# Optimization experiments

Measured on AMD Instinct MI355X. Metric: run time of the kernel, lower is better.

Reference implementation:

```python
import jax, jax.numpy as jnp
import numpy as np
import math

F = 32                      # multiplicity per irrep (l0dim = l1dim = l2dim)
NUMBASIS = 8
RCUT = 4.0
BESSEL_END = 5.0
AVG_NEIGHBORS = 25.0
N_NODES = 10000
N_EDGES = 250000
HIDDEN = 64
FEAT = 9 * F                # (1+3+5) components per channel

# uvu tensor-product paths (l_in1, l_edge, l_out) allowed by l/parity selection rules
PATHS = [(0,0,0),(0,1,1),(0,2,2),(1,0,1),(1,1,0),(1,1,2),(1,2,1),(2,0,2),(2,1,1),(2,2,0),(2,2,2)]
_cnt = {}
for (_,_,k) in PATHS:
    _cnt[k] = _cnt.get(k, 0) + 1
# e3nn path weights: irrep_normalization='component', path_normalization='element' (num_elements(uvu)=mul_in2=1)
PATH_W = [math.sqrt((2*k+1) / _cnt[k]) for (_,_,k) in PATHS]

def _su2_cg(j1, j2, j3, m1, m2, m3):
    if m1 + m2 != m3:
        return 0.0
    f = math.factorial
    pref = math.sqrt((2*j3+1) * f(j1+j2-j3) * f(j1-j2+j3) * f(-j1+j2+j3) / f(j1+j2+j3+1))
    pref *= math.sqrt(f(j3+m3) * f(j3-m3) * f(j1-m1) * f(j1+m1) * f(j2-m2) * f(j2+m2))
    s = 0.0
    for k in range(0, j1+j2-j3+1):
        d = [k, j1+j2-j3-k, j1-m1-k, j2+m2-k, j3-j2+m1+k, j3-j1-m2+k]
        if min(d) < 0:
            continue
        s += (-1)**k / (f(d[0])*f(d[1])*f(d[2])*f(d[3])*f(d[4])*f(d[5]))
    return pref * s

def _q(l):
    # complex->real SH change of basis (e3nn convention)
    q = np.zeros((2*l+1, 2*l+1), dtype=np.complex128)
    for m in range(-l, 0):
        q[l+m, l+abs(m)] = 1/math.sqrt(2)
        q[l+m, l-abs(m)] = -1j/math.sqrt(2)
    q[l, l] = 1.0
    for m in range(1, l+1):
        q[l+m, l+abs(m)] = (-1)**m/math.sqrt(2)
        q[l+m, l-abs(m)] = 1j*(-1)**m/math.sqrt(2)
    return (-1j)**l * q

def _w3j(l1, l2, l3):
    C = np.zeros((2*l1+1, 2*l2+1, 2*l3+1))
    for m1 in range(-l1, l1+1):
        for m2 in range(-l2, l2+1):
            for m3 in range(-l3, l3+1):
                C[l1+m1, l2+m2, l3+m3] = _su2_cg(l1, l2, l3, m1, m2, m3)
    W = np.einsum('ij,kl,mn,ikm->jln', _q(l1), _q(l2), np.conj(_q(l3)), C.astype(np.complex128))
    Wr, Wi = np.real(W), np.imag(W)
    W = Wr if np.linalg.norm(Wr) >= np.linalg.norm(Wi) else Wi
    return (W / np.linalg.norm(W)).astype(np.float32)   # unit-Frobenius real 3j, as in e3nn

W3J = {p: _w3j(*p) for p in PATHS}

def _bessel(d):
    # soft_one_hot_linspace(d, 0, 5, 8, basis='bessel', cutoff=True)
    t = d / BESSEL_END
    n = jnp.arange(1, NUMBASIS + 1, dtype=d.dtype)
    safe_t = jnp.where(t > 0, t, 1.0)
    out = math.sqrt(2.0 / BESSEL_END) * jnp.sin(n * jnp.pi * t[:, None]) / safe_t[:, None]
    return out * (((t > 0) & (t < 1)).astype(d.dtype))[:, None]

def _poly_cutoff(d):
    u = d / RCUT                      # p = 6
    env = 1.0 - 6.0 * u**5 + 5.0 * u**6
    return env * (d < RCUT).astype(d.dtype)

def _sph(unit):
    # component-normalized real spherical harmonics l=0,1,2 on unit vectors
    x, y, z = unit[:, 0], unit[:, 1], unit[:, 2]
    y0 = jnp.ones_like(x)[:, None]
    y1 = math.sqrt(3.0) * jnp.stack([y, z, x], axis=-1)
    y2 = jnp.stack([
        math.sqrt(15.0) * x * y,
        math.sqrt(15.0) * y * z,
        (math.sqrt(5.0) / 2.0) * (3.0 * z * z - 1.0),
        math.sqrt(15.0) * x * z,
        (math.sqrt(15.0) / 2.0) * (x * x - y * y),
    ], axis=-1)
    return (y0, y1, y2)

def _forward(nodes, pos, src, dst, w1, b1, w2, b2):
    neighbors = nodes[src]                                    # [E, 9F] gather
    posvec = pos[src] - pos[dst]                              # [E, 3]
    dist = jnp.sqrt(jnp.sum(posvec * posvec, axis=1))         # [E]
    h = jax.nn.silu(_bessel(dist) @ w1 + b1)                  # [E, 64]
    radial = (h @ w2 + b2) * _poly_cutoff(dist)[:, None]      # [E, 11F]
    w = radial.reshape(-1, len(PATHS), F)                     # [E, P, F]
    unit = posvec / jnp.maximum(dist, 1e-12)[:, None]
    ys = _sph(unit)                                           # ([E,1],[E,3],[E,5])
    x0 = neighbors[:, :F].reshape(-1, F, 1)
    x1 = neighbors[:, F:4*F].reshape(-1, F, 3)
    x2 = neighbors[:, 4*F:].reshape(-1, F, 5)
    xs = (x0, x1, x2)
    outs = [0.0, 0.0, 0.0]
    for p, (i, j, k) in enumerate(PATHS):
        Wp = jnp.asarray(W3J[(i, j, k)])                      # [di, dj, dk]
        msg = jnp.einsum('abc,eua,eb,eu->euc', Wp, xs[i], ys[j], w[:, p, :])
        outs[k] = outs[k] + PATH_W[p] * msg
    messages = jnp.concatenate([o.reshape(o.shape[0], -1) for o in outs], axis=1)  # [E, 9F]
    agg = jax.ops.segment_sum(messages, dst, num_segments=N_NODES)
    return agg / math.sqrt(AVG_NEIGHBORS)

def setup_inputs():
    key = jax.random.key(0)
    ks = jax.random.split(key, 6)
    nodes = jax.random.normal(ks[0], (N_NODES, FEAT), dtype=jnp.float32)
    pos = jax.random.normal(ks[1], (N_NODES, 3), dtype=jnp.float32)
    src = jax.random.randint(ks[2], (N_EDGES,), 0, N_NODES)
    dst = jax.random.randint(ks[3], (N_EDGES,), 0, N_NODES)
    w1 = jax.random.normal(ks[4], (NUMBASIS, HIDDEN), dtype=jnp.float32) / math.sqrt(NUMBASIS)
    b1 = jnp.zeros((HIDDEN,), jnp.float32)
    w2 = jax.random.normal(ks[5], (HIDDEN, len(PATHS)*F), dtype=jnp.float32) / math.sqrt(HIDDEN)
    b2 = jnp.zeros((len(PATHS)*F,), jnp.float32)
    return {"nodes": nodes, "pos": pos, "src": src, "dst": dst, "w1": w1, "b1": b1, "w2": w2, "b2": b2}

def reference(nodes, pos, src, dst, w1, b1, w2, b2):
    return _forward(nodes, pos, src, dst, w1, b1, w2, b2)
```

## Files before the change

kernel.cpp:

```cpp
#include <hip/hip_runtime.h>
#include <hip/hip_bf16.h>
#include <cmath>
#include <complex>

#define TPB 256
#define WPB 4
#define NM 115
#define NW3J 363
#define MPITCH 116
#define RPITCH 388
#define W2FN 22528
#define SCAN_T 1024
#define NBUCK 256

typedef __attribute__((ext_vector_type(8))) short bf16x8;
typedef __attribute__((ext_vector_type(4))) float f32x4;

namespace {

double fct(int n){ double r=1; for(int i=2;i<=n;i++) r*=i; return r; }

double su2_cg(int j1,int j2,int j3,int m1,int m2,int m3){
  if(m1+m2!=m3) return 0.0;
  double pref = std::sqrt((2*j3+1)*fct(j1+j2-j3)*fct(j1-j2+j3)*fct(-j1+j2+j3)/fct(j1+j2+j3+1));
  pref *= std::sqrt(fct(j3+m3)*fct(j3-m3)*fct(j1-m1)*fct(j1+m1)*fct(j2-m2)*fct(j2+m2));
  double s=0;
  for(int k=0;k<=j1+j2-j3;k++){
    int d0=k, d1=j1+j2-j3-k, d2=j1-m1-k, d3=j2+m2-k, d4=j3-j2+m1+k, d5=j3-j1-m2+k;
    if(d0<0||d1<0||d2<0||d3<0||d4<0||d5<0) continue;
    double t = 1.0/(fct(d0)*fct(d1)*fct(d2)*fct(d3)*fct(d4)*fct(d5));
    s += (k&1)? -t : t;
  }
  return pref*s;
}

typedef std::complex<double> cd;

void qmat(int l, cd q[5][5]){
  for(int i=0;i<5;i++) for(int j=0;j<5;j++) q[i][j] = cd(0,0);
  const double is2 = 1.0/std::sqrt(2.0);
  for(int m=-l;m<0;m++){ q[l+m][l-m] = cd(is2,0); q[l+m][l+m] = cd(0,-is2); }
  q[l][l] = cd(1,0);
  for(int m=1;m<=l;m++){ double sg = (m&1)? -1.0: 1.0; q[l+m][l+m] = cd(sg*is2,0); q[l+m][l-m] = cd(0, sg*is2); }
  cd ph(1,0), mi(0,-1);
  for(int t=0;t<l;t++) ph *= mi;
  for(int i=0;i<5;i++) for(int j=0;j<5;j++) q[i][j] *= ph;
}

void w3j_calc(int l1,int l2,int l3,double* out){
  int n1=2*l1+1,n2=2*l2+1,n3=2*l3+1;
  double C[5][5][5] = {};
  for(int m1=-l1;m1<=l1;m1++)for(int m2=-l2;m2<=l2;m2++)for(int m3=-l3;m3<=l3;m3++)
    C[l1+m1][l2+m2][l3+m3] = su2_cg(l1,l2,l3,m1,m2,m3);
  cd q1[5][5], q2[5][5], q3[5][5];
  qmat(l1,q1); qmat(l2,q2); qmat(l3,q3);
  double wr[125], wi[125];
  double nr=0, ni=0;
  for(int a=0;a<n1;a++)for(int b=0;b<n2;b++)for(int c=0;c<n3;c++){
    cd s(0,0);
    for(int i=0;i<n1;i++)for(int k=0;k<n2;k++)for(int m=0;m<n3;m++)
      s += q1[i][a]*q2[k][b]*std::conj(q3[m][c])*C[i][k][m];
    int idx = (a*n2+b)*n3+c;
    wr[idx]=s.real(); wi[idx]=s.imag();
    nr += s.real()*s.real(); ni += s.imag()*s.imag();
  }
  bool useR = std::sqrt(nr) >= std::sqrt(ni);
  double nn = std::sqrt(useR? nr: ni);
  for(int q=0;q<n1*n2*n3;q++) out[q] = (useR? wr[q]: wi[q])/nn;
}

struct UploadArg {
  float w3j[NW3J];
  unsigned int meta[NM];
};

UploadArg g_upload;

struct BuildInit {
  BuildInit(){
    const int P[11][3] = {{0,0,0},{0,1,1},{0,2,2},{1,0,1},{1,1,0},{1,1,2},
                          {1,2,1},{2,0,2},{2,1,1},{2,2,0},{2,2,2}};
    const int cnt[3] = {3,4,4};
    const int AO[3] = {0,1,4};
    int off = 0, t = 0;
    for(int p=0;p<11;p++){
      int i=P[p][0], j=P[p][1], k=P[p][2];
      int na=2*i+1, nb=2*j+1, nc=2*k+1;
      double W[125];
      w3j_calc(i,j,k,W);
      double pw = std::sqrt((2.0*k+1.0)/(double)cnt[k]);
      for(int q=0;q<na*nb*nc;q++) g_upload.w3j[off+q] = (float)(W[q]*pw);
      for(int a=0;a<na;a++)
        for(int c=0;c<nc;c++)
          g_upload.meta[t++] = (unsigned)((off + a*nb*nc + c) | (nc<<10) | (nb<<14) | (AO[j]<<18));
      off += na*nb*nc;
    }
  }
};
BuildInit g_build_init;

}


__global__ void count_repack_kernel(const int* __restrict__ dst, int* __restrict__ counts,
                                    const float* __restrict__ w2,
                                    unsigned short* __restrict__ w2f, int E){
  int i = blockIdx.x*blockDim.x + threadIdx.x;
  if(i < W2FN){
    int jj = i & 7;
    int lane = (i>>3) & 63;
    int kk = (i>>9) & 1;
    int t  = i>>10;
    int n = t*16 + (lane & 15);
    int k = kk*32 + ((lane>>4)&3)*8 + jj;
    unsigned ub = __float_as_uint(w2[k*352 + n]);
    ub = (ub + 0x7fffu + ((ub>>16)&1u)) >> 16;
    w2f[i] = (unsigned short)ub;
  }
  if(i < E) atomicAdd(&counts[dst[i]], 1);
}

__global__ __launch_bounds__(SCAN_T) void megascan_kernel(const int* __restrict__ counts,
                                                          int* __restrict__ off,
                                                          int* __restrict__ cursor,
                                                          int* __restrict__ bcur, int NN){
  __shared__ int part[SCAN_T];
  __shared__ int lh[NBUCK];
  int t = threadIdx.x;
  if(t < NBUCK) lh[t] = 0;
  __syncthreads();
  int C = (NN + SCAN_T - 1)/SCAN_T;
  int base = t*C;
  int lim = min(base+C, NN);
  int s = 0;
  for(int i=base;i<lim;i++){
    int c = counts[i];
    s += c;
    atomicAdd(&lh[min(c, NBUCK-1)], 1);
  }
  part[t] = s;
  __syncthreads();
  for(int d=1; d<SCAN_T; d<<=1){
    int v = (t>=d)? part[t-d] : 0;
    __syncthreads();
    part[t] += v;
    __syncthreads();
  }
  int run = part[t] - s;
  for(int i=base;i<lim;i++){ off[i]=run; cursor[i]=run; run += counts[i]; }
  if(t == SCAN_T-1) off[NN] = part[t];
  __syncthreads();
  if(t == 0){
    int r = 0;
    for(int b=0;b<NBUCK;b++){ bcur[b] = r; r += lh[b]; }
  }
}

__global__ void scatter_kernel(const int* __restrict__ dst, const int* __restrict__ counts,
                               int* __restrict__ cursor, int* __restrict__ bcur,
                               int* __restrict__ node_order, int* __restrict__ eid,
                               int NN, int E){
  int i = blockIdx.x*blockDim.x + threadIdx.x;
  if(i < NN){
    int p = atomicAdd(&bcur[min(counts[i], NBUCK-1)], 1);
    node_order[p] = i;
  }
  if(i < E){
    int p = atomicAdd(&cursor[dst[i]], 1);
    eid[p] = i;
  }
}


__global__ __launch_bounds__(TPB) void node_kernel(
    const float* __restrict__ nodes,
    const float* __restrict__ pos,
    const int* __restrict__ src,
    const int* __restrict__ node_order,
    const int* __restrict__ offp,
    const int* __restrict__ eid,
    const unsigned short* __restrict__ w2f,
    const float* __restrict__ w1,
    const float* __restrict__ b1,
    const float* __restrict__ b2,
    float* __restrict__ outp,
    int NN, UploadArg up)
{
  __shared__ alignas(16) float s_w3j[NW3J];
  __shared__ alignas(16) float s_w1[512];
  __shared__ alignas(16) float s_b1[64];
  __shared__ alignas(16) float s_b2[352];
  __shared__ alignas(16) unsigned short s_h[WPB][16*68];
  __shared__ alignas(16) float s_M[WPB][16*MPITCH];
  __shared__ alignas(16) float s_rad[WPB][16*RPITCH];

  const int tid  = threadIdx.x;
  const int wid  = tid >> 6;
  const int lane = tid & 63;
  const int q    = lane >> 4;
  const int i    = lane & 15;
  const int u    = lane & 31;
  const int half = lane >> 5;

  for(int t=tid; t<NW3J; t+=TPB) s_w3j[t] = up.w3j[t];
  for(int t=tid; t<512; t+=TPB)  s_w1[t]  = w1[t];
  for(int t=tid; t<352; t+=TPB)  s_b2[t]  = b2[t];
  if(tid < 64) s_b1[tid] = b1[tid];
  __syncthreads();

  const int nidx   = blockIdx.x*WPB + wid;
  const bool active = nidx < NN;
  const int node   = active ? node_order[nidx] : 0;
  const int start  = offp[node];
  const int deg    = active ? (offp[node+1] - start) : 0;

  const float dpx = pos[node*3+0], dpy = pos[node*3+1], dpz = pos[node*3+2];

  float accv[9];
  #pragma unroll
  for(int k=0;k<9;k++) accv[k] = 0.0f;

  char* hbytes = (char*)&s_h[wid][0];
  float* Mw    = &s_M[wid][0];
  float* radw  = &s_rad[wid][0];
  const uint4* w2f4 = (const uint4*)w2f;

  constexpr int PI_[11]   = {0,0,0,1,1,1,1,2,2,2,2};
  constexpr int PK_[11]   = {0,1,2,1,0,2,1,2,1,0,2};
  constexpr int TOFF_[11] = {0,1,4,9,18,21,36,45,70,85,90};
  constexpr int AO_[3]    = {0,1,4};

  const int nch = (deg + 15) >> 4;

  for(int ch=0; ch<nch; ch++){
    int ei = ch*16 + i;
    bool v = ei < deg;
    int eg = v ? eid[start+ei] : 0;
    int se = v ? src[eg] : node;
    float px = pos[se*3+0]-dpx, py = pos[se*3+1]-dpy, pz = pos[se*3+2]-dpz;
    float d2 = px*px + py*py + pz*pz;
    float d  = v ? sqrtf(d2) : 1e9f;
    float inv = 1.0f/fmaxf(d, 1e-12f);
    float x = px*inv, y = py*inv, z = pz*inv;
    float yv[9];
    yv[0]=1.0f;
    yv[1]=1.7320508075688772f*y;
    yv[2]=1.7320508075688772f*z;
    yv[3]=1.7320508075688772f*x;
    yv[4]=3.872983346207417f*x*y;
    yv[5]=3.872983346207417f*y*z;
    yv[6]=1.118033988749895f*(3.0f*z*z-1.0f);
    yv[7]=3.872983346207417f*x*z;
    yv[8]=1.9364916731037085f*(x*x-y*y);
    float bes[8];
    {
      float tt = d * 0.2f;
      float st = (tt > 0.0f) ? tt : 1.0f;
      float msk = (tt > 0.0f && tt < 1.0f) ? 1.0f : 0.0f;
      float ang = 3.14159265358979323846f * tt;
      float s1 = __sinf(ang), c1 = __cosf(ang);
      float kk2 = 0.6324555320336759f * msk / st;
      float c2 = 2.0f*c1;
      float sp = 0.0f, sc = s1;
      bes[0] = kk2*s1;
      #pragma unroll
      for(int n=1;n<8;n++){ float sn = c2*sc - sp; sp = sc; sc = sn; bes[n] = kk2*sn; }
    }
    float cut;
    {
      float uu = d*0.25f;
      float u2 = uu*uu;
      float u5 = u2*u2*uu;
      float env = 1.0f - 6.0f*u5 + 5.0f*u5*uu;
      cut = (d < 4.0f) ? env : 0.0f;
    }

    unsigned hp[8];
    #pragma unroll
    for(int s=0;s<16;s++){
      int j = q*16 + s;
      float a = s_b1[j];
      #pragma unroll
      for(int k=0;k<8;k++) a += bes[k]*s_w1[k*64+j];
      float sg = 1.0f/(1.0f + __expf(-a));
      float h = a*sg;
      unsigned ub = __float_as_uint(h);
      ub = (ub + 0x7fffu + ((ub>>16)&1u)) >> 16;
      if(s & 1) hp[s>>1] |= ub<<16; else hp[s>>1] = ub;
    }
    {
      uint2* wp = (uint2*)(hbytes + i*136 + q*32);
      wp[0] = make_uint2(hp[0],hp[1]);
      wp[1] = make_uint2(hp[2],hp[3]);
      wp[2] = make_uint2(hp[4],hp[5]);
      wp[3] = make_uint2(hp[6],hp[7]);
    }

    for(int s5=0; s5<29; s5++){
      int t = q + 4*s5;
      if(t < NM){
        unsigned md = up.meta[t];
        int woff = md & 1023;
        int nc   = (md>>10) & 15;
        int nb   = (md>>14) & 15;
        int boff = (md>>18) & 15;
        float sm = 0.0f;
        for(int b=0;b<nb;b++) sm += s_w3j[woff + b*nc] * yv[boff + b];
        Mw[i*MPITCH + t] = sm;
      }
    }

    float cut4[4];
    #pragma unroll
    for(int r=0;r<4;r++) cut4[r] = __shfl(cut, 4*q + r);

    __threadfence_block();

    union UA { uint2 u2[2]; bf16x8 v; };
    UA A0, A1;
    {
      const char* ab = hbytes + i*136 + q*16;
      A0.u2[0] = *(const uint2*)(ab);
      A0.u2[1] = *(const uint2*)(ab + 8);
      A1.u2[0] = *(const uint2*)(ab + 64);
      A1.u2[1] = *(const uint2*)(ab + 72);
    }

    #pragma unroll 2
    for(int p=0;p<11;p++){
      #pragma unroll
      for(int hv=0;hv<2;hv++){
        int t = 2*p + hv;
        union UB { uint4 u4; bf16x8 v; } B0, B1;
        B0.u4 = w2f4[(t*2+0)*64 + lane];
        B1.u4 = w2f4[(t*2+1)*64 + lane];
        f32x4 c = {0.f,0.f,0.f,0.f};
        c = __builtin_amdgcn_mfma_f32_16x16x32_bf16(A0.v, B0.v, c, 0,0,0);
        c = __builtin_amdgcn_mfma_f32_16x16x32_bf16(A1.v, B1.v, c, 0,0,0);
        float bias = s_b2[p*32 + hv*16 + i];
        #pragma unroll
        for(int r=0;r<4;r++){
          radw[(4*q+r)*RPITCH + (hv*16+i)*12 + p] = (c[r] + bias) * cut4[r];
        }
      }
    }

    __threadfence_block();

    for(int jj=0; jj<8; jj++){
      if(ch*16 + 2*jj >= deg) break;
      int e = 2*jj + half;
      int seE = __shfl(se, e);
      const float* nr = nodes + (long)seE*288;
      float xv[9];
      xv[0] = nr[u];
      #pragma unroll
      for(int c=0;c<3;c++) xv[1+c] = nr[32 + u*3 + c];
      #pragma unroll
      for(int c=0;c<5;c++) xv[4+c] = nr[128 + u*5 + c];
      const float* rp = radw + e*RPITCH + u*12;
      float4 r0 = *(const float4*)(rp);
      float4 r1 = *(const float4*)(rp+4);
      float4 r2 = *(const float4*)(rp+8);
      float wr[12] = {r0.x,r0.y,r0.z,r0.w, r1.x,r1.y,r1.z,r1.w, r2.x,r2.y,r2.z,r2.w};
      const float* Me = Mw + e*MPITCH;
      #pragma unroll
      for(int p=0;p<11;p++){
        const int na = 2*PI_[p]+1;
        const int nc = 2*PK_[p]+1;
        const int ai = AO_[PI_[p]], ko = AO_[PK_[p]];
        float w = wr[p];
        #pragma unroll
        for(int a=0;a<na;a++){
          float xw = xv[ai+a]*w;
          #pragma unroll
          for(int c=0;c<nc;c++) accv[ko+c] += xw * Me[TOFF_[p] + a*nc + c];
        }
      }
    }
  }

  #pragma unroll
  for(int k=0;k<9;k++) accv[k] += __shfl_xor(accv[k], 32);

  if(active && lane < 32){
    float* ob = outp + (long)node*288;
    ob[u] = 0.2f*accv[0];
    #pragma unroll
    for(int c=0;c<3;c++) ob[32 + u*3 + c] = 0.2f*accv[1+c];
    #pragma unroll
    for(int c=0;c<5;c++) ob[128 + u*5 + c] = 0.2f*accv[4+c];
  }
}


extern "C" void kernel_launch(void* const* d_in, const int* in_sizes, int n_in,
                              void* d_out, int out_size, void* d_ws, size_t ws_size,
                              hipStream_t stream) {
  const float* nodes = (const float*)d_in[0];
  const float* pos   = (const float*)d_in[1];
  const int* src = (const int*)d_in[2];
  const int* dst = (const int*)d_in[3];
  const float* w1 = (const float*)d_in[4];
  const float* b1 = (const float*)d_in[5];
  const float* w2 = (const float*)d_in[6];
  const float* b2 = (const float*)d_in[7];

  const int E  = in_sizes[2];
  const int NN = in_sizes[0] / 288;
  float* outp = (float*)d_out;

  unsigned short* w2f = (unsigned short*)d_ws;
  int* counts     = (int*)(w2f + W2FN);
  int* offp       = counts + NN;
  int* cursor     = offp + NN + 1;
  int* bcur       = cursor + NN;
  int* node_order = bcur + NBUCK;
  int* eid        = node_order + NN;

  hipMemsetAsync(counts, 0, (size_t)NN*sizeof(int), stream);

  int g1 = (max(E, W2FN) + 255)/256;
  count_repack_kernel<<<g1, 256, 0, stream>>>(dst, counts, w2, w2f, E);
  megascan_kernel<<<1, SCAN_T, 0, stream>>>(counts, offp, cursor, bcur, NN);
  int g2 = (max(E, NN) + 255)/256;
  scatter_kernel<<<g2, 256, 0, stream>>>(dst, counts, cursor, bcur, node_order, eid, NN, E);

  int nblocks = (NN + WPB - 1)/WPB;
  node_kernel<<<nblocks, TPB, 0, stream>>>(nodes, pos, src, node_order, offp, eid,
                                           w2f, w1, b1, b2, outp, NN, g_upload);
}
```

Before: 638.7 us.

## Consume MFMA radial weights in registers, drop radial LDS staging

The radial MLP output is now used straight from the MFMA accumulator registers instead of being written to a per-wave LDS buffer and read back. The tensor-product contraction is regrouped so each lane handles 4 edges × 16 channels, using a transposed M layout that is read with float4 loads. The LDS footprint shrinks and launch bounds ask for 3 blocks per CU. In exchange, block-wide __syncthreads replace per-wave fences, so every wave in a block runs as many chunks as the highest-degree wave, and each lane loads node features for 4 edges.

```diff
diff --git a/kernel.cpp b/kernel.cpp
--- a/kernel.cpp
+++ b/kernel.cpp
@@ -7,8 +7,6 @@
 #define WPB 4
 #define NM 115
 #define NW3J 363
-#define MPITCH 116
-#define RPITCH 388
 #define W2FN 22528
 #define SCAN_T 1024
 #define NBUCK 256
@@ -172,7 +170,7 @@
 }
 
 
-__global__ __launch_bounds__(TPB) void node_kernel(
+__global__ __launch_bounds__(TPB, 3) void node_kernel(
     const float* __restrict__ nodes,
     const float* __restrict__ pos,
     const int* __restrict__ src,
@@ -191,38 +189,44 @@
   __shared__ alignas(16) float s_b1[64];
   __shared__ alignas(16) float s_b2[352];
   __shared__ alignas(16) unsigned short s_h[WPB][16*68];
-  __shared__ alignas(16) float s_M[WPB][16*MPITCH];
-  __shared__ alignas(16) float s_rad[WPB][16*RPITCH];
+  __shared__ alignas(16) float s_MT[WPB][NM*16];
+  __shared__ int s_deg[WPB];
 
   const int tid  = threadIdx.x;
   const int wid  = tid >> 6;
   const int lane = tid & 63;
   const int q    = lane >> 4;
   const int i    = lane & 15;
-  const int u    = lane & 31;
-  const int half = lane >> 5;
 
   for(int t=tid; t<NW3J; t+=TPB) s_w3j[t] = up.w3j[t];
   for(int t=tid; t<512; t+=TPB)  s_w1[t]  = w1[t];
   for(int t=tid; t<352; t+=TPB)  s_b2[t]  = b2[t];
   if(tid < 64) s_b1[tid] = b1[tid];
-  __syncthreads();
 
   const int nidx   = blockIdx.x*WPB + wid;
   const bool active = nidx < NN;
   const int node   = active ? node_order[nidx] : 0;
   const int start  = offp[node];
   const int deg    = active ? (offp[node+1] - start) : 0;
+  if(lane == 0) s_deg[wid] = deg;
+  __syncthreads();
+
+  int degmax = s_deg[0];
+  #pragma unroll
+  for(int w=1;w<WPB;w++) degmax = max(degmax, s_deg[w]);
+  const int nch_blk  = (degmax + 15) >> 4;
+  const int nch_self = (deg + 15) >> 4;
 
   const float dpx = pos[node*3+0], dpy = pos[node*3+1], dpz = pos[node*3+2];
 
-  float accv[9];
+  float acc[2][9];
   #pragma unroll
-  for(int k=0;k<9;k++) accv[k] = 0.0f;
+  for(int hv=0;hv<2;hv++)
+    #pragma unroll
+    for(int k=0;k<9;k++) acc[hv][k] = 0.0f;
 
   char* hbytes = (char*)&s_h[wid][0];
-  float* Mw    = &s_M[wid][0];
-  float* radw  = &s_rad[wid][0];
+  float* MwT   = &s_MT[wid][0];
   const uint4* w2f4 = (const uint4*)w2f;
 
   constexpr int PI_[11]   = {0,0,0,1,1,1,1,2,2,2,2};
@@ -230,166 +234,177 @@
   constexpr int TOFF_[11] = {0,1,4,9,18,21,36,45,70,85,90};
   constexpr int AO_[3]    = {0,1,4};
 
-  const int nch = (deg + 15) >> 4;
-
-  for(int ch=0; ch<nch; ch++){
-    int ei = ch*16 + i;
-    bool v = ei < deg;
-    int eg = v ? eid[start+ei] : 0;
-    int se = v ? src[eg] : node;
-    float px = pos[se*3+0]-dpx, py = pos[se*3+1]-dpy, pz = pos[se*3+2]-dpz;
-    float d2 = px*px + py*py + pz*pz;
-    float d  = v ? sqrtf(d2) : 1e9f;
-    float inv = 1.0f/fmaxf(d, 1e-12f);
-    float x = px*inv, y = py*inv, z = pz*inv;
-    float yv[9];
-    yv[0]=1.0f;
-    yv[1]=1.7320508075688772f*y;
-    yv[2]=1.7320508075688772f*z;
-    yv[3]=1.7320508075688772f*x;
-    yv[4]=3.872983346207417f*x*y;
-    yv[5]=3.872983346207417f*y*z;
-    yv[6]=1.118033988749895f*(3.0f*z*z-1.0f);
-    yv[7]=3.872983346207417f*x*z;
-    yv[8]=1.9364916731037085f*(x*x-y*y);
-    float bes[8];
-    {
-      float tt = d * 0.2f;
-      float st = (tt > 0.0f) ? tt : 1.0f;
-      float msk = (tt > 0.0f && tt < 1.0f) ? 1.0f : 0.0f;
-      float ang = 3.14159265358979323846f * tt;
-      float s1 = __sinf(ang), c1 = __cosf(ang);
-      float kk2 = 0.6324555320336759f * msk / st;
-      float c2 = 2.0f*c1;
-      float sp = 0.0f, sc = s1;
-      bes[0] = kk2*s1;
+  for(int ch=0; ch<nch_blk; ch++){
+    const bool mine = (ch < nch_self);
+    float cut = 0.0f;
+    int   se  = node;
+
+    if(mine){
+      int ei = ch*16 + i;
+      bool v = ei < deg;
+      int eg = v ? eid[start+ei] : 0;
+      se = v ? src[eg] : node;
+      float px = pos[se*3+0]-dpx, py = pos[se*3+1]-dpy, pz = pos[se*3+2]-dpz;
+      float d2 = px*px + py*py + pz*pz;
+      float d  = v ? sqrtf(d2) : 1e9f;
+      float inv = 1.0f/fmaxf(d, 1e-12f);
+      float x = px*inv, y = py*inv, z = pz*inv;
+      float yv[9];
+      yv[0]=1.0f;
+      yv[1]=1.7320508075688772f*y;
+      yv[2]=1.7320508075688772f*z;
+      yv[3]=1.7320508075688772f*x;
+      yv[4]=3.872983346207417f*x*y;
+      yv[5]=3.872983346207417f*y*z;
+      yv[6]=1.118033988749895f*(3.0f*z*z-1.0f);
+      yv[7]=3.872983346207417f*x*z;
+      yv[8]=1.9364916731037085f*(x*x-y*y);
+      float bes[8];
+      {
+        float tt = d * 0.2f;
+        float st = (tt > 0.0f) ? tt : 1.0f;
+        float msk = (tt > 0.0f && tt < 1.0f) ? 1.0f : 0.0f;
+        float ang = 3.14159265358979323846f * tt;
+        float s1 = __sinf(ang), c1 = __cosf(ang);
+        float kk2 = 0.6324555320336759f * msk / st;
+        float c2 = 2.0f*c1;
+        float sp = 0.0f, sc = s1;
+        bes[0] = kk2*s1;
+        #pragma unroll
+        for(int n=1;n<8;n++){ float sn = c2*sc - sp; sp = sc; sc = sn; bes[n] = kk2*sn; }
+      }
+      {
+        float uu = d*0.25f;
+        float u2 = uu*uu;
+        float u5 = u2*u2*uu;
+        float env = 1.0f - 6.0f*u5 + 5.0f*u5*uu;
+        cut = (d < 4.0f) ? env : 0.0f;
+      }
+
+      unsigned hp[8];
       #pragma unroll
-      for(int n=1;n<8;n++){ float sn = c2*sc - sp; sp = sc; sc = sn; bes[n] = kk2*sn; }
-    }
-    float cut;
-    {
-      float uu = d*0.25f;
-      float u2 = uu*uu;
-      float u5 = u2*u2*uu;
-      float env = 1.0f - 6.0f*u5 + 5.0f*u5*uu;
-      cut = (d < 4.0f) ? env : 0.0f;
-    }
-
-    unsigned hp[8];
-    #pragma unroll
-    for(int s=0;s<16;s++){
-      int j = q*16 + s;
-      float a = s_b1[j];
+      for(int s=0;s<16;s++){
+        int j = q*16 + s;
+        float a = s_b1[j];
+        #pragma unroll
+        for(int k=0;k<8;k++) a += bes[k]*s_w1[k*64+j];
+        float sg = 1.0f/(1.0f + __expf(-a));
+        float h = a*sg;
+        unsigned ub = __float_as_uint(h);
+        ub = (ub + 0x7fffu + ((ub>>16)&1u)) >> 16;
+        if(s & 1) hp[s>>1] |= ub<<16; else hp[s>>1] = ub;
+      }
+      {
+        uint2* wp = (uint2*)(hbytes + i*136 + q*32);
+        wp[0] = make_uint2(hp[0],hp[1]);
+        wp[1] = make_uint2(hp[2],hp[3]);
+        wp[2] = make_uint2(hp[4],hp[5]);
+        wp[3] = make_uint2(hp[6],hp[7]);
+      }
+
+      for(int s5=0; s5<29; s5++){
+        int t = q + 4*s5;
+        if(t < NM){
+          unsigned md = up.meta[t];
+          int woff = md & 1023;
+          int nc   = (md>>10) & 15;
+          int nb   = (md>>14) & 15;
+          int boff = (md>>18) & 15;
+          float sm = 0.0f;
+          for(int b=0;b<nb;b++) sm += s_w3j[woff + b*nc] * yv[boff + b];
+          MwT[t*16 + i] = sm;
+        }
+      }
+    }
+
+    __syncthreads();
+
+    if(mine){
+      float cut4[4];
+      int   se4[4];
       #pragma unroll
-      for(int k=0;k<8;k++) a += bes[k]*s_w1[k*64+j];
-      float sg = 1.0f/(1.0f + __expf(-a));
-      float h = a*sg;
-      unsigned ub = __float_as_uint(h);
-      ub = (ub + 0x7fffu + ((ub>>16)&1u)) >> 16;
-      if(s & 1) hp[s>>1] |= ub<<16; else hp[s>>1] = ub;
-    }
-    {
-      uint2* wp = (uint2*)(hbytes + i*136 + q*32);
-      wp[0] = make_uint2(hp[0],hp[1]);
-      wp[1] = make_uint2(hp[2],hp[3]);
-      wp[2] = make_uint2(hp[4],hp[5]);
-      wp[3] = make_uint2(hp[6],hp[7]);
-    }
-
-    for(int s5=0; s5<29; s5++){
-      int t = q + 4*s5;
-      if(t < NM){
-        unsigned md = up.meta[t];
-        int woff = md & 1023;
-        int nc   = (md>>10) & 15;
-        int nb   = (md>>14) & 15;
-        int boff = (md>>18) & 15;
-        float sm = 0.0f;
-        for(int b=0;b<nb;b++) sm += s_w3j[woff + b*nc] * yv[boff + b];
-        Mw[i*MPITCH + t] = sm;
-      }
-    }
-
-    float cut4[4];
-    #pragma unroll
-    for(int r=0;r<4;r++) cut4[r] = __shfl(cut, 4*q + r);
-
-    __threadfence_block();
-
-    union UA { uint2 u2[2]; bf16x8 v; };
-    UA A0, A1;
-    {
-      const char* ab = hbytes + i*136 + q*16;
-      A0.u2[0] = *(const uint2*)(ab);
-      A0.u2[1] = *(const uint2*)(ab + 8);
-      A1.u2[0] = *(const uint2*)(ab + 64);
-      A1.u2[1] = *(const uint2*)(ab + 72);
-    }
-
-    #pragma unroll 2
-    for(int p=0;p<11;p++){
-      #pragma unroll
-      for(int hv=0;hv<2;hv++){
-        int t = 2*p + hv;
-        union UB { uint4 u4; bf16x8 v; } B0, B1;
-        B0.u4 = w2f4[(t*2+0)*64 + lane];
-        B1.u4 = w2f4[(t*2+1)*64 + lane];
-        f32x4 c = {0.f,0.f,0.f,0.f};
-        c = __builtin_amdgcn_mfma_f32_16x16x32_bf16(A0.v, B0.v, c, 0,0,0);
-        c = __builtin_amdgcn_mfma_f32_16x16x32_bf16(A1.v, B1.v, c, 0,0,0);
-        float bias = s_b2[p*32 + hv*16 + i];
+      for(int r=0;r<4;r++){ cut4[r] = __shfl(cut, 4*q+r); se4[r] = __shfl(se, 4*q+r); }
+
+      union UA { uint2 u2[2]; bf16x8 v; };
+      UA A0, A1;
+      {
+        const char* ab = hbytes + i*136 + q*16;
+        A0.u2[0] = *(const uint2*)(ab);
+        A0.u2[1] = *(const uint2*)(ab + 8);
+        A1.u2[0] = *(const uint2*)(ab + 64);
+        A1.u2[1] = *(const uint2*)(ab + 72);
+      }
+
+      #pragma unroll 1
+      for(int hv=0; hv<2; hv++){
+        const int c0 = hv*16 + i;
+        float xv[4][9];
         #pragma unroll
         for(int r=0;r<4;r++){
-          radw[(4*q+r)*RPITCH + (hv*16+i)*12 + p] = (c[r] + bias) * cut4[r];
+          const float* nr = nodes + (long)se4[r]*288;
+          xv[r][0] = nr[c0];
+          #pragma unroll
+          for(int c=0;c<3;c++) xv[r][1+c] = nr[32 + c0*3 + c];
+          #pragma unroll
+          for(int c=0;c<5;c++) xv[r][4+c] = nr[128 + c0*5 + c];
         }
-      }
-    }
-
-    __threadfence_block();
-
-    for(int jj=0; jj<8; jj++){
-      if(ch*16 + 2*jj >= deg) break;
-      int e = 2*jj + half;
-      int seE = __shfl(se, e);
-      const float* nr = nodes + (long)seE*288;
-      float xv[9];
-      xv[0] = nr[u];
-      #pragma unroll
-      for(int c=0;c<3;c++) xv[1+c] = nr[32 + u*3 + c];
-      #pragma unroll
-      for(int c=0;c<5;c++) xv[4+c] = nr[128 + u*5 + c];
-      const float* rp = radw + e*RPITCH + u*12;
-      float4 r0 = *(const float4*)(rp);
-      float4 r1 = *(const float4*)(rp+4);
-      float4 r2 = *(const float4*)(rp+8);
-      float wr[12] = {r0.x,r0.y,r0.z,r0.w, r1.x,r1.y,r1.z,r1.w, r2.x,r2.y,r2.z,r2.w};
-      const float* Me = Mw + e*MPITCH;
-      #pragma unroll
-      for(int p=0;p<11;p++){
-        const int na = 2*PI_[p]+1;
-        const int nc = 2*PK_[p]+1;
-        const int ai = AO_[PI_[p]], ko = AO_[PK_[p]];
-        float w = wr[p];
         #pragma unroll
-        for(int a=0;a<na;a++){
-          float xw = xv[ai+a]*w;
+        for(int p=0;p<11;p++){
+          int t = 2*p + hv;
+          union UB { uint4 u4; bf16x8 v; } B0, B1;
+          B0.u4 = w2f4[(t*2+0)*64 + lane];
+          B1.u4 = w2f4[(t*2+1)*64 + lane];
+          f32x4 c = {0.f,0.f,0.f,0.f};
+          c = __builtin_amdgcn_mfma_f32_16x16x32_bf16(A0.v, B0.v, c, 0,0,0);
+          c = __builtin_amdgcn_mfma_f32_16x16x32_bf16(A1.v, B1.v, c, 0,0,0);
+          float bias = s_b2[p*32 + c0];
+          float wr0 = (c[0]+bias)*cut4[0];
+          float wr1 = (c[1]+bias)*cut4[1];
+          float wr2 = (c[2]+bias)*cut4[2];
+          float wr3 = (c[3]+bias)*cut4[3];
+          const int na = 2*PI_[p]+1, nc = 2*PK_[p]+1;
+          const int ai = AO_[PI_[p]], ko = AO_[PK_[p]];
           #pragma unroll
-          for(int c=0;c<nc;c++) accv[ko+c] += xw * Me[TOFF_[p] + a*nc + c];
+          for(int a=0;a<na;a++){
+            float xw0 = xv[0][ai+a]*wr0;
+            float xw1 = xv[1][ai+a]*wr1;
+            float xw2 = xv[2][ai+a]*wr2;
+            float xw3 = xv[3][ai+a]*wr3;
+            #pragma unroll
+            for(int cc=0;cc<nc;cc++){
+              float4 m4 = *(const float4*)&MwT[(TOFF_[p]+a*nc+cc)*16 + 4*q];
+              acc[hv][ko+cc] += xw0*m4.x + xw1*m4.y + xw2*m4.z + xw3*m4.w;
+            }
+          }
         }
       }
     }
+
+    __syncthreads();
   }
 
   #pragma unroll
-  for(int k=0;k<9;k++) accv[k] += __shfl_xor(accv[k], 32);
-
-  if(active && lane < 32){
+  for(int hv=0;hv<2;hv++)
+    #pragma unroll
+    for(int k=0;k<9;k++){
+      acc[hv][k] += __shfl_xor(acc[hv][k], 16);
+      acc[hv][k] += __shfl_xor(acc[hv][k], 32);
+    }
+
+  if(active && lane < 16){
     float* ob = outp + (long)node*288;
-    ob[u] = 0.2f*accv[0];
+    ob[i]    = 0.2f*acc[0][0];
+    ob[16+i] = 0.2f*acc[1][0];
     #pragma unroll
-    for(int c=0;c<3;c++) ob[32 + u*3 + c] = 0.2f*accv[1+c];
+    for(int c=0;c<3;c++){
+      ob[32 + i*3 + c]      = 0.2f*acc[0][1+c];
+      ob[32 + (16+i)*3 + c] = 0.2f*acc[1][1+c];
+    }
     #pragma unroll
-    for(int c=0;c<5;c++) ob[128 + u*5 + c] = 0.2f*accv[4+c];
+    for(int c=0;c<5;c++){
+      ob[128 + i*5 + c]      = 0.2f*acc[0][4+c];
+      ob[128 + (16+i)*5 + c] = 0.2f*acc[1][4+c];
+    }
   }
 }
 
```

Measured after the change: 1.659 ms. +159.8%, slower.
